# Kernel tuning notes

Hardware: AMD Instinct MI355X
Metric: run time of the kernel (lower is better)

The kernel has to match this reference:

```python
import jax, jax.numpy as jnp
import numpy as np

NF, NLOC, NNEI = 4, 2048, 64
EMBED, PAIR_DIM, H = 128, 64, 8
HD = EMBED // H
EPS = 1e-5

def _ln(x, g, b):
    m = x.mean(-1, keepdims=True)
    v = ((x - m) ** 2).mean(-1, keepdims=True)
    return (x - m) * jax.lax.rsqrt(v + EPS) * g + b

def setup_inputs() -> dict:
    key = jax.random.key(0)
    ks = jax.random.split(key, 12)
    inp = {
        "query": jax.random.normal(ks[0], (NF, NLOC, EMBED), jnp.float32),
        "pair": jax.random.normal(ks[1], (NF, NLOC, NNEI, PAIR_DIM), jnp.float32),
        "nlist": jax.random.randint(ks[2], (NF, NLOC, NNEI), 0, NLOC, jnp.int64),
        "delta_pos": jax.random.normal(ks[3], (NF, NLOC, NNEI, 3), jnp.float32),
        "attn_mask": jnp.zeros((NF, H, NLOC, NNEI), jnp.float32),
        "ln_g": jnp.ones((EMBED,), jnp.float32),
        "ln_b": jnp.zeros((EMBED,), jnp.float32),
        "pn_g": jnp.ones((PAIR_DIM,), jnp.float32),
        "pn_b": jnp.zeros((PAIR_DIM,), jnp.float32),
        "Wq": jax.random.normal(ks[4], (EMBED, EMBED), jnp.float32) * (EMBED ** -0.5),
        "Wk": jax.random.normal(ks[5], (EMBED, EMBED), jnp.float32) * (EMBED ** -0.5),
        "Wv": jax.random.normal(ks[6], (EMBED, EMBED), jnp.float32) * (EMBED ** -0.5),
        "Wbias": jax.random.normal(ks[7], (H, PAIR_DIM), jnp.float32) * (PAIR_DIM ** -0.5),
        "bbias": jnp.zeros((H,), jnp.float32),
        "Wforce": jax.random.normal(ks[8], (1, EMBED), jnp.float32) * (EMBED ** -0.5),
    }
    return inp

def reference(query, pair, nlist, delta_pos, attn_mask,
              ln_g, ln_b, pn_g, pn_b, Wq, Wk, Wv, Wbias, bbias, Wforce):
    nf, nloc, _ = query.shape
    nnei = nlist.shape[-1]
    qn = _ln(query, ln_g, ln_b)            # [f,l,e]
    pn = _ln(pair, pn_g, pn_b)             # [f,l,n,p]
    scaling = HD ** -0.5
    q = (qn @ Wq.T).reshape(nf, nloc, H, HD) * scaling       # [f,l,h,d]
    k = qn @ Wk.T                                            # [f,l,e]
    v = qn @ Wv.T
    idx = nlist.reshape(nf, -1)[..., None]                   # [f,l*n,1]
    kg = jnp.take_along_axis(k, idx, axis=1).reshape(nf, nloc, nnei, H, HD)
    vg = jnp.take_along_axis(v, idx, axis=1).reshape(nf, nloc, nnei, H, HD)
    attn = jnp.einsum('flhd,flnhd->fhln', q, kg)             # [f,h,l,n]
    bias = jnp.einsum('flnp,hp->fhln', pn, Wbias) + bbias[None, :, None, None]
    probs = jax.nn.softmax(attn + attn_mask + bias, axis=-1)  # dropout off (eval)
    # rotate by delta_pos and contract with v over neighbors
    x = jnp.einsum('fhln,flnc,flnhd->flchd', probs, delta_pos, vg)
    x = x.reshape(nf, nloc, 3, EMBED)
    force = (x @ Wforce.T).squeeze(-1)                       # [f,l,3]
    return force
```

## Files before the change

### kernel.cpp

```cpp
#include <hip/hip_runtime.h>

#define NFR   4
#define NLOCC 2048
#define NNEIN 64
#define EMB   128
#define PDIM  64
#define NH    8
#define LNEPS 1e-5f
#define NROW  (NFR*NLOCC)

#define WS_Q   0
#define WS_K   (NROW*EMB)
#define WS_FV  (2*NROW*EMB)
#define WS_G   (2*NROW*EMB + NROW*NH)

__device__ __forceinline__ void fma4(float4& acc, const float4 a, const float4 b) {
    acc.x = fmaf(a.x, b.x, acc.x);
    acc.y = fmaf(a.y, b.y, acc.y);
    acc.z = fmaf(a.z, b.z, acc.z);
    acc.w = fmaf(a.w, b.w, acc.w);
}
__device__ __forceinline__ void fma4s(float4& acc, const float s, const float4 b) {
    acc.x = fmaf(s, b.x, acc.x);
    acc.y = fmaf(s, b.y, acc.y);
    acc.z = fmaf(s, b.z, acc.z);
    acc.w = fmaf(s, b.w, acc.w);
}
__device__ __forceinline__ float hsum4(const float4 a) {
    return (a.x + a.y) + (a.z + a.w);
}
__device__ __forceinline__ float dot4(const float4 a, const float4 b) {
    return fmaf(a.x, b.x, fmaf(a.y, b.y, fmaf(a.z, b.z, a.w * b.w)));
}
__device__ __forceinline__ float4 scale4(const float4 a, const float s) {
    return make_float4(a.x*s, a.y*s, a.z*s, a.w*s);
}

template<int CTRL>
__device__ __forceinline__ float dppf(float x) {
    return __int_as_float(__builtin_amdgcn_update_dpp(
        0, __float_as_int(x), CTRL, 0xF, 0xF, true));
}

__global__ __launch_bounds__(256, 2) void qkfv_kernel(
    const float* __restrict__ query,
    const float* __restrict__ ln_g, const float* __restrict__ ln_b,
    const float* __restrict__ Wq, const float* __restrict__ Wk,
    const float* __restrict__ Wv, const float* __restrict__ Wforce,
    const float* __restrict__ pn_g, const float* __restrict__ pn_b,
    const float* __restrict__ Wbias, const float* __restrict__ bbias,
    float* __restrict__ ws)
{
    __shared__ float  gb_s[2][EMB];
    __shared__ float  qn_s[16*132];
    __shared__ float  wt_s[2][16*132];
    __shared__ float4 wvf_s4[8*33];
    const int t = threadIdx.x;
    const int rowbase = blockIdx.x * 16;

    if (t < 64) {
        const float* src = (t < 32) ? ln_g : ln_b;
        ((float4*)gb_s[t >> 5])[t & 31] = ((const float4*)src)[t & 31];
    }

    if (blockIdx.x == 0) {
        if (t < 128) {
            const float4 wb4 = ((const float4*)Wbias)[t];
            const float4 pg4 = ((const float4*)pn_g)[t & 15];
            ((float4*)(ws + WS_G))[t] =
                make_float4(wb4.x*pg4.x, wb4.y*pg4.y, wb4.z*pg4.z, wb4.w*pg4.w);
        } else if (t < 192) {
            const int h = (t - 128) >> 3, s8 = (t - 128) & 7;
            float sg = 0.f, cb = 0.f;
            #pragma unroll
            for (int k = 0; k < 8; ++k) {
                const int p = s8*8 + k;
                const float wb = Wbias[h*PDIM + p];
                sg = fmaf(pn_g[p], wb, sg);
                cb = fmaf(pn_b[p], wb, cb);
            }
            sg += __shfl_xor(sg, 1, 64); sg += __shfl_xor(sg, 2, 64); sg += __shfl_xor(sg, 4, 64);
            cb += __shfl_xor(cb, 1, 64); cb += __shfl_xor(cb, 2, 64); cb += __shfl_xor(cb, 4, 64);
            if (s8 == 0) {
                ws[WS_G + 512 + h] = sg;
                ws[WS_G + 520 + h] = cb + bbias[h];
            }
        }
    }

    {
        const int h = t >> 5, ch = t & 31;
        float4 acc = make_float4(0.f, 0.f, 0.f, 0.f);
        #pragma unroll
        for (int d = 0; d < 16; ++d) {
            const float wf = Wforce[h*16 + d];
            const float4 wv = ((const float4*)(Wv + (size_t)(h*16 + d)*EMB))[ch];
            fma4s(acc, wf, wv);
        }
        wvf_s4[h*33 + ch] = acc;
    }

    const int r   = t >> 4;
    const int seg = t & 15;
    float4 x0 = ((const float4*)query)[(size_t)(rowbase + r)*32 + seg*2 + 0];
    float4 x1 = ((const float4*)query)[(size_t)(rowbase + r)*32 + seg*2 + 1];
    float s  = (x0.x + x0.y) + (x0.z + x0.w) + (x1.x + x1.y) + (x1.z + x1.w);
    float ss = x0.x*x0.x + x0.y*x0.y + x0.z*x0.z + x0.w*x0.w
             + x1.x*x1.x + x1.y*x1.y + x1.z*x1.z + x1.w*x1.w;
    #pragma unroll
    for (int m = 1; m < 16; m <<= 1) {
        s  += __shfl_xor(s,  m, 64);
        ss += __shfl_xor(ss, m, 64);
    }
    const float mean = s * (1.0f / 128.0f);
    const float var  = ss * (1.0f / 128.0f) - mean * mean;
    const float rstd = rsqrtf(var + LNEPS);
    __syncthreads();

    {
        const int c0 = seg * 8;
        float4 o0, o1;
        o0.x = (x0.x - mean)*rstd*gb_s[0][c0+0] + gb_s[1][c0+0];
        o0.y = (x0.y - mean)*rstd*gb_s[0][c0+1] + gb_s[1][c0+1];
        o0.z = (x0.z - mean)*rstd*gb_s[0][c0+2] + gb_s[1][c0+2];
        o0.w = (x0.w - mean)*rstd*gb_s[0][c0+3] + gb_s[1][c0+3];
        o1.x = (x1.x - mean)*rstd*gb_s[0][c0+4] + gb_s[1][c0+4];
        o1.y = (x1.y - mean)*rstd*gb_s[0][c0+5] + gb_s[1][c0+5];
        o1.z = (x1.z - mean)*rstd*gb_s[0][c0+6] + gb_s[1][c0+6];
        o1.w = (x1.w - mean)*rstd*gb_s[0][c0+7] + gb_s[1][c0+7];
        ((float4*)qn_s)[r*33 + seg*2 + 0] = o0;
        ((float4*)qn_s)[r*33 + seg*2 + 1] = o1;
    }
    __syncthreads();

    const int rp = t >> 5;
    const int r0 = rp * 2;
    const int cq = t & 31;
    const int sc0 = t >> 2;
    const int si0 = t & 3;
    const float4* qn4 = (const float4*)qn_s;

    for (int w = 0; w < 2; ++w) {
        const float4* W4 = (const float4*)((w == 0) ? Wq : Wk);
        float4 acc0 = make_float4(0.f,0.f,0.f,0.f);
        float4 acc1 = make_float4(0.f,0.f,0.f,0.f);
        {
            float4 g0 = W4[(size_t)sc0*32 + si0];
            float4 g1 = W4[(size_t)(sc0+64)*32 + si0];
            float* wt = wt_s[0];
            wt[(si0*4+0)*132 + sc0] = g0.x; wt[(si0*4+1)*132 + sc0] = g0.y;
            wt[(si0*4+2)*132 + sc0] = g0.z; wt[(si0*4+3)*132 + sc0] = g0.w;
            wt[(si0*4+0)*132 + sc0+64] = g1.x; wt[(si0*4+1)*132 + sc0+64] = g1.y;
            wt[(si0*4+2)*132 + sc0+64] = g1.z; wt[(si0*4+3)*132 + sc0+64] = g1.w;
        }
        __syncthreads();
        #pragma unroll
        for (int tau = 0; tau < 8; ++tau) {
            const int buf = tau & 1;
            float4 ng0, ng1;
            if (tau < 7) {
                ng0 = W4[(size_t)sc0*32 + (tau+1)*4 + si0];
                ng1 = W4[(size_t)(sc0+64)*32 + (tau+1)*4 + si0];
            }
            const float4* wt4 = (const float4*)wt_s[buf];
            #pragma unroll
            for (int e4 = 0; e4 < 4; ++e4) {
                float4 a0 = qn4[r0*33 + tau*4 + e4];
                float4 a1 = qn4[(r0+1)*33 + tau*4 + e4];
                const float* a0p = (const float*)&a0;
                const float* a1p = (const float*)&a1;
                #pragma unroll
                for (int ee = 0; ee < 4; ++ee) {
                    const float4 wv = wt4[(e4*4+ee)*33 + cq];
                    fma4s(acc0, a0p[ee], wv);
                    fma4s(acc1, a1p[ee], wv);
                }
            }
            if (tau < 7) {
                float* wt = wt_s[buf ^ 1];
                wt[(si0*4+0)*132 + sc0] = ng0.x; wt[(si0*4+1)*132 + sc0] = ng0.y;
                wt[(si0*4+2)*132 + sc0] = ng0.z; wt[(si0*4+3)*132 + sc0] = ng0.w;
                wt[(si0*4+0)*132 + sc0+64] = ng1.x; wt[(si0*4+1)*132 + sc0+64] = ng1.y;
                wt[(si0*4+2)*132 + sc0+64] = ng1.z; wt[(si0*4+3)*132 + sc0+64] = ng1.w;
            }
            __syncthreads();
        }
        const float sc = (w == 0) ? 0.25f : 1.0f;
        float4* dst = (float4*)(ws + (w == 0 ? WS_Q : WS_K));
        dst[(size_t)(rowbase + r0)*32 + cq]     = scale4(acc0, sc);
        dst[(size_t)(rowbase + r0 + 1)*32 + cq] = scale4(acc1, sc);
    }

    if (t < 128) {
        const int rr = t >> 3, h = t & 7;
        float4 acc = make_float4(0.f,0.f,0.f,0.f);
        #pragma unroll
        for (int ch = 0; ch < 32; ++ch)
            fma4(acc, qn4[rr*33 + ch], wvf_s4[h*33 + ch]);
        ws[WS_FV + (size_t)(rowbase + rr)*NH + h] = hsum4(acc);
    }
}

__global__ __launch_bounds__(256, 3) void attn_force_kernel(
    const float* __restrict__ pair, const int* __restrict__ nlist,
    const float* __restrict__ delta_pos, const float* __restrict__ attn_mask,
    const float* __restrict__ ws, float* __restrict__ out)
{
    __shared__ float  logit_s[NNEIN*9];
    __shared__ float  bias_s[NNEIN*9];
    __shared__ float  fv_s[NNEIN*9];
    __shared__ float  dp_s[192];
    __shared__ float4 gw_s4[4*128];
    __shared__ float  fpart[4][3];

    const int t    = threadIdx.x;
    const int bid  = blockIdx.x;
    const int fr   = bid >> 11;
    const int l    = bid & (NLOCC - 1);
    const int w    = t >> 6;
    const int lane = t & 63;
    const int n    = t >> 2;
    const int sub  = t & 3;
    const int half = lane >> 5;
    const int c    = lane & 31;
    const int hh   = t >> 5;
    const int i32  = lane & 31;

    int jr[8];
    #pragma unroll
    for (int i = 0; i < 8; ++i)
        jr[i] = nlist[(size_t)bid*NNEIN + ((w << 4) | (i << 1) | half)];
    const int jn = nlist[(size_t)bid*NNEIN + n];

    const float4 q4c = ((const float4*)(ws + WS_Q))[(size_t)bid*32 + c];

    const size_t mbase = (((size_t)(fr*NH + hh))*NLOCC + l)*NNEIN;
    const float ma = attn_mask[mbase + i32];
    const float mb = attn_mask[mbase + i32 + 32];

    const float4* pr4 = (const float4*)(pair + ((size_t)bid*NNEIN + n)*PDIM) + sub*4;
    const float4 p0 = pr4[0];
    const float4 p1 = pr4[1];
    const float4 p2 = pr4[2];
    const float4 p3 = pr4[3];

    {
        const float4* Gg = (const float4*)(ws + WS_G);
        gw_s4[(w << 7) | lane]        = Gg[lane];
        gw_s4[(w << 7) | (64 + lane)] = Gg[64 + lane];
    }

    if (t >= 192 && t < 240)
        ((float4*)dp_s)[t - 192] = ((const float4*)(delta_pos + (size_t)bid*192))[t - 192];

    const float4* k4 = (const float4*)(ws + WS_K) + (size_t)(fr << 11)*32;
    float4 kk[8];
    #pragma unroll
    for (int i = 0; i < 8; ++i) kk[i] = k4[(size_t)jr[i]*32 + c];

    {
        const float2 fv2 = ((const float2*)(ws + WS_FV + ((size_t)(fr << 11) + jn)*NH))[sub];
        fv_s[n*9 + sub*2]     = fv2.x;
        fv_s[n*9 + sub*2 + 1] = fv2.y;
    }

    {
        #pragma unroll
        for (int i = 0; i < 8; ++i) {
            float pp = dot4(kk[i], q4c);
            pp += dppf<0xB1>(pp);
            pp += dppf<0x4E>(pp);
            if ((c & 3) == 0)
                logit_s[((w << 4) | (i << 1) | half)*9 + (c >> 2)] = pp;
        }
    }

    {
        float s  = hsum4(p0) + hsum4(p1) + hsum4(p2) + hsum4(p3);
        float ss = dot4(p0,p0) + dot4(p1,p1) + dot4(p2,p2) + dot4(p3,p3);
        s  += dppf<0xB1>(s);  s  += dppf<0x4E>(s);
        ss += dppf<0xB1>(ss); ss += dppf<0x4E>(ss);

        float d[NH];
        #pragma unroll
        for (int h = 0; h < NH; ++h) d[h] = 0.f;
        const float4* gw = &gw_s4[w << 7];
        const float4 prq[4] = {p0, p1, p2, p3};
        #pragma unroll
        for (int q = 0; q < 4; ++q) {
            #pragma unroll
            for (int h = 0; h < NH; ++h)
                d[h] += dot4(prq[q], gw[h*16 + sub*4 + q]);
        }
        #pragma unroll
        for (int h = 0; h < NH; ++h) {
            d[h] += dppf<0xB1>(d[h]);
            d[h] += dppf<0x4E>(d[h]);
        }
        const float mean = s * (1.0f / 64.0f);
        const float var  = ss * (1.0f / 64.0f) - mean * mean;
        const float rstd = rsqrtf(var + LNEPS);
        const float* SGp = ws + WS_G + 512;
        const int h0 = sub*2, h1 = h0 + 1;
        bias_s[n*9 + h0] = rstd*(d[h0] - mean*SGp[h0]) + SGp[8 + h0];
        bias_s[n*9 + h1] = rstd*(d[h1] - mean*SGp[h1]) + SGp[8 + h1];
    }
    __syncthreads();

    {
        const float a = logit_s[i32*9 + hh]        + bias_s[i32*9 + hh]        + ma;
        const float b = logit_s[(i32 + 32)*9 + hh] + bias_s[(i32 + 32)*9 + hh] + mb;
        float m = fmaxf(a, b);
        m = fmaxf(m, __shfl_xor(m, 16, 64));
        m = fmaxf(m, __shfl_xor(m,  8, 64));
        m = fmaxf(m, __shfl_xor(m,  4, 64));
        m = fmaxf(m, dppf<0x4E>(m));
        m = fmaxf(m, dppf<0xB1>(m));
        const float ea = __expf(a - m), eb = __expf(b - m);
        float sum = ea + eb;
        sum += __shfl_xor(sum, 16, 64);
        sum += __shfl_xor(sum,  8, 64);
        sum += __shfl_xor(sum,  4, 64);
        sum += dppf<0x4E>(sum);
        sum += dppf<0xB1>(sum);
        const float inv = 1.0f / sum;
        const float ca = ea * inv * fv_s[i32*9 + hh];
        const float cb = eb * inv * fv_s[(i32 + 32)*9 + hh];

        const float dpax = dp_s[i32*3 + 0],      dpay = dp_s[i32*3 + 1],      dpaz = dp_s[i32*3 + 2];
        const float dpbx = dp_s[(i32+32)*3 + 0], dpby = dp_s[(i32+32)*3 + 1], dpbz = dp_s[(i32+32)*3 + 2];
        float f0 = ca*dpax + cb*dpbx;
        float f1 = ca*dpay + cb*dpby;
        float f2 = ca*dpaz + cb*dpbz;
        f0 += dppf<0x111>(f0); f0 += dppf<0x112>(f0); f0 += dppf<0x114>(f0); f0 += dppf<0x118>(f0);
        f0 += dppf<0x142>(f0); f0 += dppf<0x143>(f0);
        f1 += dppf<0x111>(f1); f1 += dppf<0x112>(f1); f1 += dppf<0x114>(f1); f1 += dppf<0x118>(f1);
        f1 += dppf<0x142>(f1); f1 += dppf<0x143>(f1);
        f2 += dppf<0x111>(f2); f2 += dppf<0x112>(f2); f2 += dppf<0x114>(f2); f2 += dppf<0x118>(f2);
        f2 += dppf<0x142>(f2); f2 += dppf<0x143>(f2);
        if (lane == 63) {
            fpart[w][0] = f0; fpart[w][1] = f1; fpart[w][2] = f2;
        }
    }
    __syncthreads();

    if (t < 3)
        out[(size_t)bid*3 + t] = fpart[0][t] + fpart[1][t] + fpart[2][t] + fpart[3][t];
}

extern "C" void kernel_launch(void* const* d_in, const int* in_sizes, int n_in,
                              void* d_out, int out_size, void* d_ws, size_t ws_size,
                              hipStream_t stream) {
    const float* query     = (const float*)d_in[0];
    const float* pair      = (const float*)d_in[1];
    const int*   nlist     = (const int*)d_in[2];
    const float* delta_pos = (const float*)d_in[3];
    const float* attn_mask = (const float*)d_in[4];
    const float* ln_g      = (const float*)d_in[5];
    const float* ln_b      = (const float*)d_in[6];
    const float* pn_g      = (const float*)d_in[7];
    const float* pn_b      = (const float*)d_in[8];
    const float* Wq        = (const float*)d_in[9];
    const float* Wk        = (const float*)d_in[10];
    const float* Wv        = (const float*)d_in[11];
    const float* Wbias     = (const float*)d_in[12];
    const float* bbias     = (const float*)d_in[13];
    const float* Wforce    = (const float*)d_in[14];
    float* out = (float*)d_out;
    float* ws  = (float*)d_ws;

    qkfv_kernel<<<512, 256, 0, stream>>>(query, ln_g, ln_b, Wq, Wk, Wv, Wforce,
                                         pn_g, pn_b, Wbias, bbias, ws);
    attn_force_kernel<<<NROW, 256, 0, stream>>>(pair, nlist, delta_pos, attn_mask,
                                                ws, out);
}
```

Measured before the change: 255.0 us.

## Process four rows per block with double-buffered software prefetch of next row's loads

Each block now handles four consecutive atom rows instead of one. The independent loads (nlist, q, mask, pair, delta_pos) and the dependent K/fv gathers for the next row are issued while the current row computes. This hides global-memory latency, amortizes the Wbias-table shared-memory staging, and removes the delta_pos shared buffer. In exchange it raises register pressure under the 3-blocks-per-CU launch bound and quarters the grid size.

```diff
diff --git a/kernel.cpp b/kernel.cpp
--- a/kernel.cpp
+++ b/kernel.cpp
@@ -201,6 +201,31 @@
     }
 }
 
+#define ISSUE_INDEP(slot, rrow)                                                     \
+    {                                                                               \
+        _Pragma("unroll")                                                           \
+        for (int i = 0; i < 8; ++i)                                                 \
+            jr[slot][i] = nlist[(size_t)(rrow)*NNEIN + ((w << 4) | (i << 1) | half)];\
+        jn[slot] = nlist[(size_t)(rrow)*NNEIN + n];                                 \
+        q4[slot] = ((const float4*)(ws + WS_Q))[(size_t)(rrow)*32 + c];             \
+        const size_t mbase = (((size_t)(fr*NH + hh))*NLOCC + ((rrow) & (NLOCC-1)))*NNEIN; \
+        ma[slot] = attn_mask[mbase + i32];                                          \
+        mb[slot] = attn_mask[mbase + i32 + 32];                                     \
+        const float4* prp = (const float4*)(pair + ((size_t)(rrow)*NNEIN + n)*PDIM) + sub*4; \
+        pr[slot][0] = prp[0]; pr[slot][1] = prp[1];                                 \
+        pr[slot][2] = prp[2]; pr[slot][3] = prp[3];                                 \
+        const float* dpp_ = delta_pos + (size_t)(rrow)*192;                         \
+        dpa[slot][0] = dpp_[i32*3+0]; dpa[slot][1] = dpp_[i32*3+1]; dpa[slot][2] = dpp_[i32*3+2]; \
+        dpb[slot][0] = dpp_[(i32+32)*3+0]; dpb[slot][1] = dpp_[(i32+32)*3+1]; dpb[slot][2] = dpp_[(i32+32)*3+2]; \
+    }
+
+#define ISSUE_GATHER(slot)                                                          \
+    {                                                                               \
+        _Pragma("unroll")                                                           \
+        for (int i = 0; i < 8; ++i) kk[i] = k4[(size_t)jr[slot][i]*32 + c];         \
+        fv2[slot] = ((const float2*)(fvb + (size_t)jn[slot]*NH))[sub];              \
+    }
+
 __global__ __launch_bounds__(256, 3) void attn_force_kernel(
     const float* __restrict__ pair, const int* __restrict__ nlist,
     const float* __restrict__ delta_pos, const float* __restrict__ attn_mask,
@@ -209,14 +234,12 @@
     __shared__ float  logit_s[NNEIN*9];
     __shared__ float  bias_s[NNEIN*9];
     __shared__ float  fv_s[NNEIN*9];
-    __shared__ float  dp_s[192];
     __shared__ float4 gw_s4[4*128];
     __shared__ float  fpart[4][3];
 
     const int t    = threadIdx.x;
-    const int bid  = blockIdx.x;
-    const int fr   = bid >> 11;
-    const int l    = bid & (NLOCC - 1);
+    const int row0 = blockIdx.x << 2;
+    const int fr   = row0 >> 11;
     const int w    = t >> 6;
     const int lane = t & 63;
     const int n    = t >> 2;
@@ -226,126 +249,119 @@
     const int hh   = t >> 5;
     const int i32  = lane & 31;
 
-    int jr[8];
-    #pragma unroll
-    for (int i = 0; i < 8; ++i)
-        jr[i] = nlist[(size_t)bid*NNEIN + ((w << 4) | (i << 1) | half)];
-    const int jn = nlist[(size_t)bid*NNEIN + n];
-
-    const float4 q4c = ((const float4*)(ws + WS_Q))[(size_t)bid*32 + c];
-
-    const size_t mbase = (((size_t)(fr*NH + hh))*NLOCC + l)*NNEIN;
-    const float ma = attn_mask[mbase + i32];
-    const float mb = attn_mask[mbase + i32 + 32];
-
-    const float4* pr4 = (const float4*)(pair + ((size_t)bid*NNEIN + n)*PDIM) + sub*4;
-    const float4 p0 = pr4[0];
-    const float4 p1 = pr4[1];
-    const float4 p2 = pr4[2];
-    const float4 p3 = pr4[3];
-
     {
         const float4* Gg = (const float4*)(ws + WS_G);
         gw_s4[(w << 7) | lane]        = Gg[lane];
         gw_s4[(w << 7) | (64 + lane)] = Gg[64 + lane];
     }
 
-    if (t >= 192 && t < 240)
-        ((float4*)dp_s)[t - 192] = ((const float4*)(delta_pos + (size_t)bid*192))[t - 192];
-
-    const float4* k4 = (const float4*)(ws + WS_K) + (size_t)(fr << 11)*32;
+    int    jr[2][8];
+    int    jn[2];
+    float4 q4[2];
+    float  ma[2], mb[2];
+    float4 pr[2][4];
+    float  dpa[2][3], dpb[2][3];
+    float2 fv2[2];
     float4 kk[8];
+
+    const float4* k4  = (const float4*)(ws + WS_K) + (size_t)(fr << 11)*32;
+    const float*  fvb = ws + WS_FV + ((size_t)(fr << 11))*NH;
+
+    ISSUE_INDEP(0, row0);
+    ISSUE_GATHER(0);
+
     #pragma unroll
-    for (int i = 0; i < 8; ++i) kk[i] = k4[(size_t)jr[i]*32 + c];
-
-    {
-        const float2 fv2 = ((const float2*)(ws + WS_FV + ((size_t)(fr << 11) + jn)*NH))[sub];
-        fv_s[n*9 + sub*2]     = fv2.x;
-        fv_s[n*9 + sub*2 + 1] = fv2.y;
-    }
-
-    {
+    for (int r = 0; r < 4; ++r) {
+        const int cur = r & 1, nxt = cur ^ 1;
+
+        fv_s[n*9 + sub*2]     = fv2[cur].x;
+        fv_s[n*9 + sub*2 + 1] = fv2[cur].y;
+
+        if (r < 3) ISSUE_INDEP(nxt, row0 + r + 1);
+
         #pragma unroll
         for (int i = 0; i < 8; ++i) {
-            float pp = dot4(kk[i], q4c);
+            float pp = dot4(kk[i], q4[cur]);
             pp += dppf<0xB1>(pp);
             pp += dppf<0x4E>(pp);
             if ((c & 3) == 0)
                 logit_s[((w << 4) | (i << 1) | half)*9 + (c >> 2)] = pp;
         }
-    }
-
-    {
-        float s  = hsum4(p0) + hsum4(p1) + hsum4(p2) + hsum4(p3);
-        float ss = dot4(p0,p0) + dot4(p1,p1) + dot4(p2,p2) + dot4(p3,p3);
-        s  += dppf<0xB1>(s);  s  += dppf<0x4E>(s);
-        ss += dppf<0xB1>(ss); ss += dppf<0x4E>(ss);
-
-        float d[NH];
-        #pragma unroll
-        for (int h = 0; h < NH; ++h) d[h] = 0.f;
-        const float4* gw = &gw_s4[w << 7];
-        const float4 prq[4] = {p0, p1, p2, p3};
-        #pragma unroll
-        for (int q = 0; q < 4; ++q) {
-            #pragma unroll
-            for (int h = 0; h < NH; ++h)
-                d[h] += dot4(prq[q], gw[h*16 + sub*4 + q]);
-        }
-        #pragma unroll
-        for (int h = 0; h < NH; ++h) {
-            d[h] += dppf<0xB1>(d[h]);
-            d[h] += dppf<0x4E>(d[h]);
-        }
-        const float mean = s * (1.0f / 64.0f);
-        const float var  = ss * (1.0f / 64.0f) - mean * mean;
-        const float rstd = rsqrtf(var + LNEPS);
-        const float* SGp = ws + WS_G + 512;
-        const int h0 = sub*2, h1 = h0 + 1;
-        bias_s[n*9 + h0] = rstd*(d[h0] - mean*SGp[h0]) + SGp[8 + h0];
-        bias_s[n*9 + h1] = rstd*(d[h1] - mean*SGp[h1]) + SGp[8 + h1];
-    }
-    __syncthreads();
-
-    {
-        const float a = logit_s[i32*9 + hh]        + bias_s[i32*9 + hh]        + ma;
-        const float b = logit_s[(i32 + 32)*9 + hh] + bias_s[(i32 + 32)*9 + hh] + mb;
-        float m = fmaxf(a, b);
-        m = fmaxf(m, __shfl_xor(m, 16, 64));
-        m = fmaxf(m, __shfl_xor(m,  8, 64));
-        m = fmaxf(m, __shfl_xor(m,  4, 64));
-        m = fmaxf(m, dppf<0x4E>(m));
-        m = fmaxf(m, dppf<0xB1>(m));
-        const float ea = __expf(a - m), eb = __expf(b - m);
-        float sum = ea + eb;
-        sum += __shfl_xor(sum, 16, 64);
-        sum += __shfl_xor(sum,  8, 64);
-        sum += __shfl_xor(sum,  4, 64);
-        sum += dppf<0x4E>(sum);
-        sum += dppf<0xB1>(sum);
-        const float inv = 1.0f / sum;
-        const float ca = ea * inv * fv_s[i32*9 + hh];
-        const float cb = eb * inv * fv_s[(i32 + 32)*9 + hh];
-
-        const float dpax = dp_s[i32*3 + 0],      dpay = dp_s[i32*3 + 1],      dpaz = dp_s[i32*3 + 2];
-        const float dpbx = dp_s[(i32+32)*3 + 0], dpby = dp_s[(i32+32)*3 + 1], dpbz = dp_s[(i32+32)*3 + 2];
-        float f0 = ca*dpax + cb*dpbx;
-        float f1 = ca*dpay + cb*dpby;
-        float f2 = ca*dpaz + cb*dpbz;
-        f0 += dppf<0x111>(f0); f0 += dppf<0x112>(f0); f0 += dppf<0x114>(f0); f0 += dppf<0x118>(f0);
-        f0 += dppf<0x142>(f0); f0 += dppf<0x143>(f0);
-        f1 += dppf<0x111>(f1); f1 += dppf<0x112>(f1); f1 += dppf<0x114>(f1); f1 += dppf<0x118>(f1);
-        f1 += dppf<0x142>(f1); f1 += dppf<0x143>(f1);
-        f2 += dppf<0x111>(f2); f2 += dppf<0x112>(f2); f2 += dppf<0x114>(f2); f2 += dppf<0x118>(f2);
-        f2 += dppf<0x142>(f2); f2 += dppf<0x143>(f2);
-        if (lane == 63) {
-            fpart[w][0] = f0; fpart[w][1] = f1; fpart[w][2] = f2;
-        }
-    }
-    __syncthreads();
-
-    if (t < 3)
-        out[(size_t)bid*3 + t] = fpart[0][t] + fpart[1][t] + fpart[2][t] + fpart[3][t];
+
+        if (r < 3) ISSUE_GATHER(nxt);
+
+        {
+            const float4 p0 = pr[cur][0], p1 = pr[cur][1];
+            const float4 p2 = pr[cur][2], p3 = pr[cur][3];
+            float s  = hsum4(p0) + hsum4(p1) + hsum4(p2) + hsum4(p3);
+            float ss = dot4(p0,p0) + dot4(p1,p1) + dot4(p2,p2) + dot4(p3,p3);
+            s  += dppf<0xB1>(s);  s  += dppf<0x4E>(s);
+            ss += dppf<0xB1>(ss); ss += dppf<0x4E>(ss);
+
+            float d[NH];
+            #pragma unroll
+            for (int h = 0; h < NH; ++h) d[h] = 0.f;
+            const float4* gw = &gw_s4[w << 7];
+            const float4 prq[4] = {p0, p1, p2, p3};
+            #pragma unroll
+            for (int q = 0; q < 4; ++q) {
+                #pragma unroll
+                for (int h = 0; h < NH; ++h)
+                    d[h] += dot4(prq[q], gw[h*16 + sub*4 + q]);
+            }
+            #pragma unroll
+            for (int h = 0; h < NH; ++h) {
+                d[h] += dppf<0xB1>(d[h]);
+                d[h] += dppf<0x4E>(d[h]);
+            }
+            const float mean = s * (1.0f / 64.0f);
+            const float var  = ss * (1.0f / 64.0f) - mean * mean;
+            const float rstd = rsqrtf(var + LNEPS);
+            const float* SGp = ws + WS_G + 512;
+            const int h0 = sub*2, h1 = h0 + 1;
+            bias_s[n*9 + h0] = rstd*(d[h0] - mean*SGp[h0]) + SGp[8 + h0];
+            bias_s[n*9 + h1] = rstd*(d[h1] - mean*SGp[h1]) + SGp[8 + h1];
+        }
+        __syncthreads();
+
+        {
+            const float a = logit_s[i32*9 + hh]        + bias_s[i32*9 + hh]        + ma[cur];
+            const float b = logit_s[(i32 + 32)*9 + hh] + bias_s[(i32 + 32)*9 + hh] + mb[cur];
+            float m = fmaxf(a, b);
+            m = fmaxf(m, __shfl_xor(m, 16, 64));
+            m = fmaxf(m, __shfl_xor(m,  8, 64));
+            m = fmaxf(m, __shfl_xor(m,  4, 64));
+            m = fmaxf(m, dppf<0x4E>(m));
+            m = fmaxf(m, dppf<0xB1>(m));
+            const float ea = __expf(a - m), eb = __expf(b - m);
+            float sum = ea + eb;
+            sum += __shfl_xor(sum, 16, 64);
+            sum += __shfl_xor(sum,  8, 64);
+            sum += __shfl_xor(sum,  4, 64);
+            sum += dppf<0x4E>(sum);
+            sum += dppf<0xB1>(sum);
+            const float inv = 1.0f / sum;
+            const float ca = ea * inv * fv_s[i32*9 + hh];
+            const float cb = eb * inv * fv_s[(i32 + 32)*9 + hh];
+
+            float f0 = ca*dpa[cur][0] + cb*dpb[cur][0];
+            float f1 = ca*dpa[cur][1] + cb*dpb[cur][1];
+            float f2 = ca*dpa[cur][2] + cb*dpb[cur][2];
+            f0 += dppf<0x111>(f0); f0 += dppf<0x112>(f0); f0 += dppf<0x114>(f0); f0 += dppf<0x118>(f0);
+            f0 += dppf<0x142>(f0); f0 += dppf<0x143>(f0);
+            f1 += dppf<0x111>(f1); f1 += dppf<0x112>(f1); f1 += dppf<0x114>(f1); f1 += dppf<0x118>(f1);
+            f1 += dppf<0x142>(f1); f1 += dppf<0x143>(f1);
+            f2 += dppf<0x111>(f2); f2 += dppf<0x112>(f2); f2 += dppf<0x114>(f2); f2 += dppf<0x118>(f2);
+            f2 += dppf<0x142>(f2); f2 += dppf<0x143>(f2);
+            if (lane == 63) {
+                fpart[w][0] = f0; fpart[w][1] = f1; fpart[w][2] = f2;
+            }
+        }
+        __syncthreads();
+
+        if (t < 3)
+            out[(size_t)(row0 + r)*3 + t] = fpart[0][t] + fpart[1][t] + fpart[2][t] + fpart[3][t];
+    }
 }
 
 extern "C" void kernel_launch(void* const* d_in, const int* in_sizes, int n_in,
@@ -371,6 +387,6 @@
 
     qkfv_kernel<<<512, 256, 0, stream>>>(query, ln_g, ln_b, Wq, Wk, Wv, Wforce,
                                          pn_g, pn_b, Wbias, bbias, ws);
-    attn_force_kernel<<<NROW, 256, 0, stream>>>(pair, nlist, delta_pos, attn_mask,
-                                                ws, out);
-}
+    attn_force_kernel<<<NROW/4, 256, 0, stream>>>(pair, nlist, delta_pos, attn_mask,
+                                                  ws, out);
+}
```

After: 289.3 us. 1.13x slower.
